# Kernel tuning notes

Hardware: AMD Instinct MI355X
Metric: run time of the kernel (lower is better)

The kernel has to match this reference:

```python
import jax, jax.numpy as jnp
import numpy as np

B, O, I, D = 8, 128, 128, 1024


def setup_inputs() -> dict:
    key = jax.random.key(0)
    ks = jax.random.split(key, 10)
    s = 1.0 / np.sqrt(2 * D)  # torch Linear default-ish scale
    return {
        "output": jax.random.normal(ks[0], (B, O, D), jnp.float32),
        "context": jax.random.normal(ks[1], (B, I, D), jnp.float32),
        "mask": jax.random.randint(ks[2], (B, I), 0, 2, jnp.int32),
        # self.w = Linear(2*dim, dim), split into the output-half and context-half
        "w_out_w": jax.random.normal(ks[3], (D, D), jnp.float32) * s,
        "w_ctx_w": jax.random.normal(ks[4], (D, D), jnp.float32) * s,
        "w_b": jax.random.normal(ks[5], (D,), jnp.float32) * s,
        # self.score = Linear(dim, 1)
        "score_w": jax.random.normal(ks[6], (D,), jnp.float32) * (1.0 / np.sqrt(D)),
        "score_b": jnp.zeros((), jnp.float32),
        # self.linear_out = Linear(2*dim, dim)
        "lin_w": jax.random.normal(ks[7], (2 * D, D), jnp.float32) * s,
        "lin_b": jax.random.normal(ks[8], (D,), jnp.float32) * s,
    }


def reference(output, context, mask, w_out_w, w_ctx_w, w_b, score_w, score_b, lin_w, lin_b):
    # Additive (Bahdanau) attention.
    # cat(out, ctx) @ W^T == out @ W1 + ctx @ W2  -> avoid [B,O,I,2D] concat.
    s_out = jnp.einsum('bod,de->boe', output, w_out_w)            # [B,O,D]
    s_ctx = jnp.einsum('bid,de->bie', context, w_ctx_w)           # [B,I,D]
    h = jax.nn.leaky_relu(s_out[:, :, None, :] + s_ctx[:, None, :, :] + w_b)  # [B,O,I,D]
    score = jnp.einsum('boid,d->boi', h, score_w) + score_b       # [B,O,I]
    score = jnp.where(mask[:, None, :] == 1, -jnp.inf, score)
    attn = jax.nn.softmax(score, axis=-1)                         # [B,O,I]
    attn_output = jnp.einsum('boi,bid->bod', attn, context)       # mix=True: bmm
    # fn=True: linear_out on cat(attn_output, output) then leaky_relu
    combined = jnp.concatenate([attn_output, output], axis=-1)    # [B,O,2D]
    attn_output = jax.nn.leaky_relu(combined @ lin_w + lin_b)     # [B,O,D]
    return attn_output, attn
```

## Files before the change

kernel.cpp:

```cpp
#include <hip/hip_runtime.h>

namespace {

constexpr int kB = 8, kO = 128, kI = 128, kD = 1024;
constexpr long kOutAttnOff = (long)kB * kO * kD;

typedef __attribute__((ext_vector_type(8))) short short8;
typedef __attribute__((ext_vector_type(4))) float f32x4;

__device__ __forceinline__ float leaky(float x) { return fmaxf(x, 0.01f * x); }

__device__ __forceinline__ short f2bf(float f) {
    unsigned u = __builtin_bit_cast(unsigned, f);
    u += 0x7FFFu + ((u >> 16) & 1u);
    return (short)(u >> 16);
}

__device__ __forceinline__ void gll16(const void* g, void* l) {
    __builtin_amdgcn_global_load_lds(
        (const __attribute__((address_space(1))) int*)g,
        (__attribute__((address_space(3))) int*)l, 16, 0, 0);
}

__global__ __launch_bounds__(256)
void conv_all(const float* __restrict__ output, const float* __restrict__ context,
              const float* __restrict__ w1, const float* __restrict__ w2,
              const float* __restrict__ lin,
              short* __restrict__ ob16, short* __restrict__ cb16,
              short* __restrict__ w1t, short* __restrict__ w2t,
              short* __restrict__ lint)
{
    __shared__ float T[64][68];
    const int bid = blockIdx.x, tid = threadIdx.x;

    if (bid < 1024) {
        const int idx = bid * 256 + tid;
        const float* src; short* dst; int i;
        if (idx < (1 << 17)) { src = output;  dst = ob16; i = idx; }
        else                 { src = context; dst = cb16; i = idx - (1 << 17); }
        const float4* s4 = (const float4*)src + (long)i * 2;
        const float4 v0 = s4[0], v1 = s4[1];
        short8 r;
        r[0] = f2bf(v0.x); r[1] = f2bf(v0.y); r[2] = f2bf(v0.z); r[3] = f2bf(v0.w);
        r[4] = f2bf(v1.x); r[5] = f2bf(v1.y); r[6] = f2bf(v1.z); r[7] = f2bf(v1.w);
        *(short8*)(dst + (long)i * 8) = r;
        return;
    }

    const int tb = bid - 1024;
    const float* src; short* dst; long C, R; int t2;
    if (tb < 256)      { src = w1;  dst = w1t;  R = 1024; C = 1024; t2 = tb; }
    else if (tb < 512) { src = w2;  dst = w2t;  R = 1024; C = 1024; t2 = tb - 256; }
    else               { src = lin; dst = lint; R = 2048; C = 1024; t2 = tb - 512; }
    const int tr = t2 >> 4, tc = t2 & 15;
    const int r = tid >> 2, q = tid & 3;

    const float* s = src + (long)(tr * 64 + r) * C + tc * 64 + q * 16;
    const float4 a0 = ((const float4*)s)[0];
    const float4 a1 = ((const float4*)s)[1];
    const float4 a2 = ((const float4*)s)[2];
    const float4 a3 = ((const float4*)s)[3];
    *(float4*)&T[r][q * 16 + 0]  = a0;
    *(float4*)&T[r][q * 16 + 4]  = a1;
    *(float4*)&T[r][q * 16 + 8]  = a2;
    *(float4*)&T[r][q * 16 + 12] = a3;
    __syncthreads();

    short8 o0, o1;
#pragma unroll
    for (int j = 0; j < 8; ++j)  o0[j] = f2bf(T[q * 16 + j][r]);
#pragma unroll
    for (int j = 0; j < 8; ++j)  o1[j] = f2bf(T[q * 16 + 8 + j][r]);
    short* dp = dst + (long)(tc * 64 + r) * R + tr * 64 + q * 16;
    *(short8*)dp       = o0;
    *((short8*)dp + 1) = o1;
}

__global__ __launch_bounds__(256)
void mm_jobs(const short* __restrict__ ob16, const short* __restrict__ cb16,
             const short* __restrict__ w1t, const short* __restrict__ w2t,
             const short* __restrict__ lint,
             const float* __restrict__ w_b, const float* __restrict__ lin_b,
             float* __restrict__ s_out, float* __restrict__ s_ctx,
             float* __restrict__ outlin, short* __restrict__ ctxlin)
{
    __shared__ short As[2][64][64];
    __shared__ short Bs[2][128][64];
    const int tid = threadIdx.x;
    const int t = blockIdx.x;
    const int lane = tid & 63, w = tid >> 6;

    const short *Ap, *Bp;
    int lda, ldb, bm, bn, ldc;
    const float* bias = nullptr;
    float* Cf = nullptr;
    short* Ch = nullptr;

    if (t < 384) {
        const int job = t >> 7, jt = t & 127;
        bm = (jt >> 3) * 64; bn = (jt & 7) * 128;
        lda = 1024; ldc = 1024;
        if (job == 0)      { Ap = ob16; Bp = w1t;         ldb = 1024; bias = w_b;   Cf = s_out;  }
        else if (job == 1) { Ap = cb16; Bp = w2t;         ldb = 1024;               Cf = s_ctx;  }
        else               { Ap = ob16; Bp = lint + 1024; ldb = 2048; bias = lin_b; Cf = outlin; }
    } else {
        const int tt = t - 384, bz = tt >> 4, tw = tt & 15;
        bm = tw * 64; bn = 0;
        Ap = lint; lda = 2048;
        Bp = cb16 + (long)bz * (kI * kD); ldb = 1024;
        Ch = ctxlin + (long)bz * (kD * kI); ldc = 128;
    }

    const int m0 = (w >> 1) * 32, n0 = (w & 1) * 64;
    const int fr = lane & 15, fcol = lane >> 4, sl = lane & 7;
    const int r8 = lane >> 3;
    const int sw8 = ((lane & 7) ^ r8) * 8;
    const int w16 = w * 16, w32 = w * 32;

    f32x4 acc[2][4] = {};

    auto stage = [&](int buf, int k0) {
        const short* ga = Ap + (long)(bm + w16 + r8) * lda + k0 + sw8;
        gll16(ga,                 &As[buf][w16][0]);
        gll16(ga + 8 * (long)lda, &As[buf][w16 + 8][0]);
        const short* gb = Bp + (long)(bn + w32 + r8) * ldb + k0 + sw8;
        gll16(gb,                  &Bs[buf][w32][0]);
        gll16(gb + 8 * (long)ldb,  &Bs[buf][w32 + 8][0]);
        gll16(gb + 16 * (long)ldb, &Bs[buf][w32 + 16][0]);
        gll16(gb + 24 * (long)ldb, &Bs[buf][w32 + 24][0]);
    };

    stage(0, 0);
    __syncthreads();
    int cur = 0;
    for (int s = 0; s < 16; ++s) {
        if (s < 15) stage(cur ^ 1, (s + 1) << 6);
#pragma unroll
        for (int ks8 = 0; ks8 < 8; ks8 += 4) {
            const int sa = ((ks8 + fcol) ^ sl) * 8;
            short8 a[2], b[4];
#pragma unroll
            for (int mi = 0; mi < 2; ++mi)
                a[mi] = *(const short8*)&As[cur][m0 + mi * 16 + fr][sa];
#pragma unroll
            for (int ni = 0; ni < 4; ++ni)
                b[ni] = *(const short8*)&Bs[cur][n0 + ni * 16 + fr][sa];
#pragma unroll
            for (int mi = 0; mi < 2; ++mi)
#pragma unroll
                for (int ni = 0; ni < 4; ++ni)
                    acc[mi][ni] = __builtin_amdgcn_mfma_f32_16x16x32_bf16(
                        a[mi], b[ni], acc[mi][ni], 0, 0, 0);
        }
        __syncthreads();
        cur ^= 1;
    }

    float bv[4] = {0, 0, 0, 0};
    if (bias) {
#pragma unroll
        for (int ni = 0; ni < 4; ++ni) bv[ni] = bias[bn + n0 + ni * 16 + fr];
    }
#pragma unroll
    for (int mi = 0; mi < 2; ++mi)
#pragma unroll
        for (int ni = 0; ni < 4; ++ni)
#pragma unroll
            for (int r = 0; r < 4; ++r) {
                const int row = bm + m0 + mi * 16 + ((lane >> 4) << 2) + r;
                const int col = bn + n0 + ni * 16 + fr;
                float v = acc[mi][ni][r] + bv[ni];
                if (Ch) Ch[(long)row * ldc + col] = f2bf(v);
                else    Cf[(long)row * ldc + col] = v;
            }
}

__global__ __launch_bounds__(256)
void score_final(const float* __restrict__ s_out, const float* __restrict__ s_ctx,
                 const float* __restrict__ score_w, const float* __restrict__ score_b,
                 const int* __restrict__ mask, const short* __restrict__ ctxlin,
                 const float* __restrict__ outlin, float* __restrict__ out_main,
                 float* __restrict__ attn_f32)
{
    __shared__ float As[4][1032];
    __shared__ __align__(16) char CsPool[65536];
    __shared__ float Wsh[1024];
    __shared__ float Ps[4][4][128];
    __shared__ float Psi[4][128];
    __shared__ float so_sh[4];
    __shared__ int   Msk[128];
    __shared__ short Pl[16][136];

    float (*Cs)[128][64] = reinterpret_cast<float(*)[128][64]>(CsPool);
    const int b   = blockIdx.x;
    const int o0  = blockIdx.y * 4;
    const int tid = threadIdx.x;
    const int wv  = tid >> 6;
    const int ln  = tid & 63;
    const int fr  = ln & 15;

    const float* arow = s_out + (long)(b * kO + o0) * kD;
#pragma unroll
    for (int q = 0; q < 4; ++q) {
        const int tq = tid + q * 256;
        const int rr = tq >> 8, c4 = (tq & 255) * 4;
        *(float4*)&As[rr][c4] = *(const float4*)&arow[(long)rr * kD + c4];
    }
    *(float4*)&Wsh[tid * 4] = *(const float4*)&score_w[tid * 4];
    if (tid < 128) Msk[tid] = mask[b * kI + tid];
    {
        short* pf = &Pl[0][0];
        for (int j = tid; j < 272; j += 256) *(short8*)(pf + j * 8) = short8{};
    }

    const float* crow = s_ctx + (long)b * kI * kD;
    const int srow = wv * 4 + (ln >> 4);
    const int cho  = ((ln & 15) ^ (srow & 7)) * 4;

    auto stageCs = [&](int buf, int dc) {
#pragma unroll
        for (int it = 0; it < 8; ++it)
            gll16(crow + (long)(srow + it * 16) * kD + dc + cho,
                  &Cs[buf][wv * 4 + it * 16][0]);
    };

    stageCs(0, 0);
    __syncthreads();

    {
        float acc = 0.0f;
#pragma unroll
        for (int j = 0; j < 16; j += 4) {
            const float4 av = *(const float4*)&As[wv][ln * 16 + j];
            const float4 ww = *(const float4*)&Wsh[ln * 16 + j];
            acc = fmaf(av.x, ww.x, acc); acc = fmaf(av.y, ww.y, acc);
            acc = fmaf(av.z, ww.z, acc); acc = fmaf(av.w, ww.w, acc);
        }
#pragma unroll
        for (int d = 1; d < 64; d <<= 1) acc += __shfl_xor(acc, d, 64);
        if (ln == 0) so_sh[wv] = acc;
    }

    float sa0[4] = {}, sa1[4] = {};
    float si0 = 0.0f, si1 = 0.0f;
    const int kb = wv * 16;

    int buf = 0;
    for (int c = 0; c < 16; ++c) {
        const int dc = c * 64;
        if (c < 15) stageCs(buf ^ 1, dc + 64);
#pragma unroll
        for (int kq = 0; kq < 4; ++kq) {
            const int sc = ((wv * 4 + kq) ^ (ln & 7)) * 4;
            const float4 c0 = *(const float4*)&Cs[buf][ln][sc];
            const float4 c1 = *(const float4*)&Cs[buf][ln + 64][sc];
            const float4 w4 = *(const float4*)&Wsh[dc + kb + kq * 4];
            si0 = fmaf(c0.x, w4.x, si0); si0 = fmaf(c0.y, w4.y, si0);
            si0 = fmaf(c0.z, w4.z, si0); si0 = fmaf(c0.w, w4.w, si0);
            si1 = fmaf(c1.x, w4.x, si1); si1 = fmaf(c1.y, w4.y, si1);
            si1 = fmaf(c1.z, w4.z, si1); si1 = fmaf(c1.w, w4.w, si1);
#pragma unroll
            for (int o = 0; o < 4; ++o) {
                const float4 av = *(const float4*)&As[o][dc + kb + kq * 4];
                sa0[o] = fmaf(__builtin_fabsf(av.x + c0.x), w4.x, sa0[o]);
                sa0[o] = fmaf(__builtin_fabsf(av.y + c0.y), w4.y, sa0[o]);
                sa0[o] = fmaf(__builtin_fabsf(av.z + c0.z), w4.z, sa0[o]);
                sa0[o] = fmaf(__builtin_fabsf(av.w + c0.w), w4.w, sa0[o]);
                sa1[o] = fmaf(__builtin_fabsf(av.x + c1.x), w4.x, sa1[o]);
                sa1[o] = fmaf(__builtin_fabsf(av.y + c1.y), w4.y, sa1[o]);
                sa1[o] = fmaf(__builtin_fabsf(av.z + c1.z), w4.z, sa1[o]);
                sa1[o] = fmaf(__builtin_fabsf(av.w + c1.w), w4.w, sa1[o]);
            }
        }
        __syncthreads();
        buf ^= 1;
    }

#pragma unroll
    for (int o = 0; o < 4; ++o) {
        Ps[wv][o][ln]      = sa0[o];
        Ps[wv][o][ln + 64] = sa1[o];
    }
    Psi[wv][ln]      = si0;
    Psi[wv][ln + 64] = si1;
    __syncthreads();

    {
        const int ow = wv;
        const float negInf = -__builtin_huge_valf();
        const float sb = score_b[0];
        const float siT0 = Psi[0][ln] + Psi[1][ln] + Psi[2][ln] + Psi[3][ln];
        const float siT1 = Psi[0][ln + 64] + Psi[1][ln + 64]
                         + Psi[2][ln + 64] + Psi[3][ln + 64];
        const float saT0 = Ps[0][ow][ln] + Ps[1][ow][ln]
                         + Ps[2][ow][ln] + Ps[3][ow][ln];
        const float saT1 = Ps[0][ow][ln + 64] + Ps[1][ow][ln + 64]
                         + Ps[2][ow][ln + 64] + Ps[3][ow][ln + 64];
        const float soV = so_sh[ow];
        float s0 = 0.505f * (soV + siT0) + 0.495f * saT0 + sb;
        float s1 = 0.505f * (soV + siT1) + 0.495f * saT1 + sb;
        if (Msk[ln]      != 0) s0 = negInf;
        if (Msk[ln + 64] != 0) s1 = negInf;

        float m = fmaxf(s0, s1);
#pragma unroll
        for (int d = 1; d < 64; d <<= 1) m = fmaxf(m, __shfl_xor(m, d, 64));
        const float e0 = __expf(s0 - m);
        const float e1 = __expf(s1 - m);
        float sum = e0 + e1;
#pragma unroll
        for (int d = 1; d < 64; d <<= 1) sum += __shfl_xor(sum, d, 64);
        const float inv = 1.0f / sum;

        const long rowoff = (long)(b * kO + o0 + ow) * kI;
        const float p0 = e0 * inv, p1 = e1 * inv;
        attn_f32[rowoff + ln]      = p0;
        attn_f32[rowoff + ln + 64] = p1;
        Pl[ow][ln]      = f2bf(p0);
        Pl[ow][ln + 64] = f2bf(p1);
    }

    short* Bsh = (short*)CsPool;
    const short* ctxb = ctxlin + (long)b * (kD * kI);
    auto stageB = [&](int half, int nc) {
        short* dst = Bsh + half * (128 * 128);
#pragma unroll
        for (int it = 0; it < 8; ++it) {
            const int rb = wv * 32 + it * 4;
            const int r  = rb + (ln >> 4);
            const int gn = nc * 128 + r;
            const int sc = (ln & 15) ^ (r & 7);
            gll16(ctxb + (long)gn * kI + sc * 8, dst + rb * 128);
        }
    };

    stageB(0, 0);
    __syncthreads();
    int half = 0;
    const int fg = ln >> 4;
    for (int nc = 0; nc < 8; ++nc) {
        if (nc < 7) stageB(half ^ 1, nc + 1);
        const short* Bc = Bsh + half * (128 * 128);
        f32x4 accT0{}, accT1{};
#pragma unroll
        for (int ks = 0; ks < 4; ++ks) {
            const short8 a = *(const short8*)&Pl[fr][ks * 32 + fg * 8];
            const int n0 = (wv * 2) * 16 + fr;
            const int n1 = (wv * 2 + 1) * 16 + fr;
            const int ch0 = ((ks * 4 + fg) ^ (n0 & 7)) * 8;
            const int ch1 = ((ks * 4 + fg) ^ (n1 & 7)) * 8;
            const short8 b0 = *(const short8*)&Bc[n0 * 128 + ch0];
            const short8 b1 = *(const short8*)&Bc[n1 * 128 + ch1];
            accT0 = __builtin_amdgcn_mfma_f32_16x16x32_bf16(a, b0, accT0, 0, 0, 0);
            accT1 = __builtin_amdgcn_mfma_f32_16x16x32_bf16(a, b1, accT1, 0, 0, 0);
        }
        if (fg == 0) {
#pragma unroll
            for (int r = 0; r < 4; ++r) {
                const long off = (long)(b * kO + o0 + r) * kD;
                const int na = nc * 128 + (wv * 2) * 16 + fr;
                const int nb = nc * 128 + (wv * 2 + 1) * 16 + fr;
                out_main[off + na] = leaky(accT0[r] + outlin[off + na]);
                out_main[off + nb] = leaky(accT1[r] + outlin[off + nb]);
            }
        }
        __syncthreads();
        half ^= 1;
    }
}

}

extern "C" void kernel_launch(void* const* d_in, const int* in_sizes, int n_in,
                              void* d_out, int out_size, void* d_ws, size_t ws_size,
                              hipStream_t stream)
{
    const float* output  = (const float*)d_in[0];
    const float* context = (const float*)d_in[1];
    const int*   mask    = (const int*)d_in[2];
    const float* w_out_w = (const float*)d_in[3];
    const float* w_ctx_w = (const float*)d_in[4];
    const float* w_b     = (const float*)d_in[5];
    const float* score_w = (const float*)d_in[6];
    const float* score_b = (const float*)d_in[7];
    const float* lin_w   = (const float*)d_in[8];
    const float* lin_b   = (const float*)d_in[9];

    float* out_main = (float*)d_out;
    float* out_attn = out_main + kOutAttnOff;
    float* s_out    = out_main;

    char* wp = (char*)d_ws;
    float* s_ctx  = (float*)wp;  wp += (size_t)4 << 20;
    short* ob16   = (short*)wp;  wp += (size_t)2 << 20;
    short* cb16   = (short*)wp;  wp += (size_t)2 << 20;
    short* w1t    = (short*)wp;  wp += (size_t)2 << 20;
    short* w2t    = (short*)wp;  wp += (size_t)2 << 20;
    short* lint   = (short*)wp;  wp += (size_t)4 << 20;
    float* outlin = (float*)wp;  wp += (size_t)4 << 20;
    short* ctxlin = (short*)wp;  wp += (size_t)2 << 20;

    const dim3 blk(256);

    hipLaunchKernelGGL(conv_all, dim3(2048), blk, 0, stream,
        output, context, w_out_w, w_ctx_w, lin_w, ob16, cb16, w1t, w2t, lint);

    hipLaunchKernelGGL(mm_jobs, dim3(512), blk, 0, stream,
        ob16, cb16, w1t, w2t, lint, w_b, lin_b, s_out, s_ctx, outlin, ctxlin);

    hipLaunchKernelGGL(score_final, dim3(8, 32), blk, 0, stream,
        s_out, s_ctx, score_w, score_b, mask, ctxlin, outlin, out_main, out_attn);
}
```

Before: 72.30 us.

## Store s_ctx as bf16 and halve output rows per score block

Measured after the change: 64.56 us. 1.12x faster.

```diff
diff --git a/kernel.cpp b/kernel.cpp
--- a/kernel.cpp
+++ b/kernel.cpp
@@ -14,6 +14,15 @@
     unsigned u = __builtin_bit_cast(unsigned, f);
     u += 0x7FFFu + ((u >> 16) & 1u);
     return (short)(u >> 16);
+}
+
+__device__ __forceinline__ void b8tof(const short8 v, float* f) {
+    const unsigned* u = (const unsigned*)&v;
+#pragma unroll
+    for (int j = 0; j < 4; ++j) {
+        f[2 * j]     = __builtin_bit_cast(float, u[j] << 16);
+        f[2 * j + 1] = __builtin_bit_cast(float, u[j] & 0xffff0000u);
+    }
 }
 
 __device__ __forceinline__ void gll16(const void* g, void* l) {
@@ -81,7 +90,7 @@
              const short* __restrict__ w1t, const short* __restrict__ w2t,
              const short* __restrict__ lint,
              const float* __restrict__ w_b, const float* __restrict__ lin_b,
-             float* __restrict__ s_out, float* __restrict__ s_ctx,
+             float* __restrict__ s_out, short* __restrict__ s_ctx16,
              float* __restrict__ outlin, short* __restrict__ ctxlin)
 {
     __shared__ short As[2][64][64];
@@ -100,9 +109,9 @@
         const int job = t >> 7, jt = t & 127;
         bm = (jt >> 3) * 64; bn = (jt & 7) * 128;
         lda = 1024; ldc = 1024;
-        if (job == 0)      { Ap = ob16; Bp = w1t;         ldb = 1024; bias = w_b;   Cf = s_out;  }
-        else if (job == 1) { Ap = cb16; Bp = w2t;         ldb = 1024;               Cf = s_ctx;  }
-        else               { Ap = ob16; Bp = lint + 1024; ldb = 2048; bias = lin_b; Cf = outlin; }
+        if (job == 0)      { Ap = ob16; Bp = w1t;         ldb = 1024; bias = w_b;   Cf = s_out;   }
+        else if (job == 1) { Ap = cb16; Bp = w2t;         ldb = 1024;               Ch = s_ctx16; }
+        else               { Ap = ob16; Bp = lint + 1024; ldb = 2048; bias = lin_b; Cf = outlin;  }
     } else {
         const int tt = t - 384, bz = tt >> 4, tw = tt & 15;
         bm = tw * 64; bn = 0;
@@ -176,32 +185,32 @@
 }
 
 __global__ __launch_bounds__(256)
-void score_final(const float* __restrict__ s_out, const float* __restrict__ s_ctx,
+void score_final(const float* __restrict__ s_out, const short* __restrict__ s_ctx16,
                  const float* __restrict__ score_w, const float* __restrict__ score_b,
                  const int* __restrict__ mask, const short* __restrict__ ctxlin,
                  const float* __restrict__ outlin, float* __restrict__ out_main,
                  float* __restrict__ attn_f32)
 {
-    __shared__ float As[4][1032];
-    __shared__ __align__(16) char CsPool[65536];
+    __shared__ float As[2][1032];
+    __shared__ __align__(16) char CsPool[32768];
     __shared__ float Wsh[1024];
-    __shared__ float Ps[4][4][128];
+    __shared__ float Ps[4][2][128];
     __shared__ float Psi[4][128];
-    __shared__ float so_sh[4];
+    __shared__ float so_sh[2];
     __shared__ int   Msk[128];
-    __shared__ short Pl[16][136];
-
-    float (*Cs)[128][64] = reinterpret_cast<float(*)[128][64]>(CsPool);
+    __shared__ __align__(16) short Pl[16][136];
+
+    short* CsS = (short*)CsPool;
     const int b   = blockIdx.x;
-    const int o0  = blockIdx.y * 4;
+    const int o0  = blockIdx.y * 2;
     const int tid = threadIdx.x;
     const int wv  = tid >> 6;
     const int ln  = tid & 63;
-    const int fr  = ln & 15;
+    const int fr  = ln & 15, fg = ln >> 4;
 
     const float* arow = s_out + (long)(b * kO + o0) * kD;
 #pragma unroll
-    for (int q = 0; q < 4; ++q) {
+    for (int q = 0; q < 2; ++q) {
         const int tq = tid + q * 256;
         const int rr = tq >> 8, c4 = (tq & 255) * 4;
         *(float4*)&As[rr][c4] = *(const float4*)&arow[(long)rr * kD + c4];
@@ -213,21 +222,21 @@
         for (int j = tid; j < 272; j += 256) *(short8*)(pf + j * 8) = short8{};
     }
 
-    const float* crow = s_ctx + (long)b * kI * kD;
-    const int srow = wv * 4 + (ln >> 4);
-    const int cho  = ((ln & 15) ^ (srow & 7)) * 4;
-
+    const short* crow = s_ctx16 + (long)b * kI * kD;
     auto stageCs = [&](int buf, int dc) {
 #pragma unroll
-        for (int it = 0; it < 8; ++it)
-            gll16(crow + (long)(srow + it * 16) * kD + dc + cho,
-                  &Cs[buf][wv * 4 + it * 16][0]);
+        for (int it = 0; it < 4; ++it) {
+            const int rb = wv * 32 + it * 8;
+            const int r  = rb + (ln >> 3);
+            const int sc = (ln & 7) ^ (r & 7);
+            gll16(crow + (long)r * kD + dc + sc * 8, CsS + buf * 8192 + rb * 64);
+        }
     };
 
     stageCs(0, 0);
     __syncthreads();
 
-    {
+    if (wv < 2) {
         float acc = 0.0f;
 #pragma unroll
         for (int j = 0; j < 16; j += 4) {
@@ -241,7 +250,7 @@
         if (ln == 0) so_sh[wv] = acc;
     }
 
-    float sa0[4] = {}, sa1[4] = {};
+    float sa0[2] = {}, sa1[2] = {};
     float si0 = 0.0f, si1 = 0.0f;
     const int kb = wv * 16;
 
@@ -249,43 +258,60 @@
     for (int c = 0; c < 16; ++c) {
         const int dc = c * 64;
         if (c < 15) stageCs(buf ^ 1, dc + 64);
-#pragma unroll
-        for (int kq = 0; kq < 4; ++kq) {
-            const int sc = ((wv * 4 + kq) ^ (ln & 7)) * 4;
-            const float4 c0 = *(const float4*)&Cs[buf][ln][sc];
-            const float4 c1 = *(const float4*)&Cs[buf][ln + 64][sc];
-            const float4 w4 = *(const float4*)&Wsh[dc + kb + kq * 4];
-            si0 = fmaf(c0.x, w4.x, si0); si0 = fmaf(c0.y, w4.y, si0);
-            si0 = fmaf(c0.z, w4.z, si0); si0 = fmaf(c0.w, w4.w, si0);
-            si1 = fmaf(c1.x, w4.x, si1); si1 = fmaf(c1.y, w4.y, si1);
-            si1 = fmaf(c1.z, w4.z, si1); si1 = fmaf(c1.w, w4.w, si1);
-#pragma unroll
-            for (int o = 0; o < 4; ++o) {
-                const float4 av = *(const float4*)&As[o][dc + kb + kq * 4];
-                sa0[o] = fmaf(__builtin_fabsf(av.x + c0.x), w4.x, sa0[o]);
-                sa0[o] = fmaf(__builtin_fabsf(av.y + c0.y), w4.y, sa0[o]);
-                sa0[o] = fmaf(__builtin_fabsf(av.z + c0.z), w4.z, sa0[o]);
-                sa0[o] = fmaf(__builtin_fabsf(av.w + c0.w), w4.w, sa0[o]);
-                sa1[o] = fmaf(__builtin_fabsf(av.x + c1.x), w4.x, sa1[o]);
-                sa1[o] = fmaf(__builtin_fabsf(av.y + c1.y), w4.y, sa1[o]);
-                sa1[o] = fmaf(__builtin_fabsf(av.z + c1.z), w4.z, sa1[o]);
-                sa1[o] = fmaf(__builtin_fabsf(av.w + c1.w), w4.w, sa1[o]);
+        const int sc0 = ((wv * 2 + 0) ^ (ln & 7)) * 8;
+        const int sc1 = ((wv * 2 + 1) ^ (ln & 7)) * 8;
+        const short8 cA0 = *(const short8*)&CsS[buf * 8192 + ln * 64 + sc0];
+        const short8 cA1 = *(const short8*)&CsS[buf * 8192 + ln * 64 + sc1];
+        const short8 cB0 = *(const short8*)&CsS[buf * 8192 + (ln + 64) * 64 + sc0];
+        const short8 cB1 = *(const short8*)&CsS[buf * 8192 + (ln + 64) * 64 + sc1];
+        float c0[16], c1[16];
+        b8tof(cA0, c0); b8tof(cA1, c0 + 8);
+        b8tof(cB0, c1); b8tof(cB1, c1 + 8);
+        float wr[16], av[2][16];
+#pragma unroll
+        for (int q = 0; q < 4; ++q) {
+            *(float4*)&wr[q * 4]    = *(const float4*)&Wsh[dc + kb + q * 4];
+            *(float4*)&av[0][q * 4] = *(const float4*)&As[0][dc + kb + q * 4];
+            *(float4*)&av[1][q * 4] = *(const float4*)&As[1][dc + kb + q * 4];
+        }
+#pragma unroll
+        for (int d = 0; d < 16; ++d) {
+            si0 = fmaf(c0[d], wr[d], si0);
+            si1 = fmaf(c1[d], wr[d], si1);
+#pragma unroll
+            for (int o = 0; o < 2; ++o) {
+                sa0[o] = fmaf(__builtin_fabsf(av[o][d] + c0[d]), wr[d], sa0[o]);
+                sa1[o] = fmaf(__builtin_fabsf(av[o][d] + c1[d]), wr[d], sa1[o]);
             }
         }
         __syncthreads();
         buf ^= 1;
     }
 
-#pragma unroll
-    for (int o = 0; o < 4; ++o) {
-        Ps[wv][o][ln]      = sa0[o];
-        Ps[wv][o][ln + 64] = sa1[o];
+    short* Bsh = (short*)CsPool;
+    const short* ctxb = ctxlin + (long)b * (kD * kI);
+    auto stageB = [&](int half, int nc) {
+#pragma unroll
+        for (int it = 0; it < 4; ++it) {
+            const int rb = wv * 16 + it * 4;
+            const int r  = rb + (ln >> 4);
+            const int n  = nc * 64 + r;
+            const int sc = (ln & 15) ^ (r & 7);
+            gll16(ctxb + (long)n * kI + sc * 8, Bsh + half * 8192 + rb * kI);
+        }
+    };
+    stageB(0, 0);
+
+#pragma unroll
+    for (int o = 0; o < 2; ++o) {
+        Ps[wv][o][ln]      = (o == 0) ? sa0[0] : sa0[1];
+        Ps[wv][o][ln + 64] = (o == 0) ? sa1[0] : sa1[1];
     }
     Psi[wv][ln]      = si0;
     Psi[wv][ln + 64] = si1;
     __syncthreads();
 
-    {
+    if (wv < 2) {
         const int ow = wv;
         const float negInf = -__builtin_huge_valf();
         const float sb = score_b[0];
@@ -319,49 +345,26 @@
         Pl[ow][ln]      = f2bf(p0);
         Pl[ow][ln + 64] = f2bf(p1);
     }
-
-    short* Bsh = (short*)CsPool;
-    const short* ctxb = ctxlin + (long)b * (kD * kI);
-    auto stageB = [&](int half, int nc) {
-        short* dst = Bsh + half * (128 * 128);
-#pragma unroll
-        for (int it = 0; it < 8; ++it) {
-            const int rb = wv * 32 + it * 4;
-            const int r  = rb + (ln >> 4);
-            const int gn = nc * 128 + r;
-            const int sc = (ln & 15) ^ (r & 7);
-            gll16(ctxb + (long)gn * kI + sc * 8, dst + rb * 128);
-        }
-    };
-
-    stageB(0, 0);
     __syncthreads();
+
     int half = 0;
-    const int fg = ln >> 4;
-    for (int nc = 0; nc < 8; ++nc) {
-        if (nc < 7) stageB(half ^ 1, nc + 1);
-        const short* Bc = Bsh + half * (128 * 128);
-        f32x4 accT0{}, accT1{};
+    for (int nc = 0; nc < 16; ++nc) {
+        if (nc < 15) stageB(half ^ 1, nc + 1);
+        const short* Bc = Bsh + half * 8192;
+        f32x4 acc{};
 #pragma unroll
         for (int ks = 0; ks < 4; ++ks) {
             const short8 a = *(const short8*)&Pl[fr][ks * 32 + fg * 8];
-            const int n0 = (wv * 2) * 16 + fr;
-            const int n1 = (wv * 2 + 1) * 16 + fr;
-            const int ch0 = ((ks * 4 + fg) ^ (n0 & 7)) * 8;
-            const int ch1 = ((ks * 4 + fg) ^ (n1 & 7)) * 8;
-            const short8 b0 = *(const short8*)&Bc[n0 * 128 + ch0];
-            const short8 b1 = *(const short8*)&Bc[n1 * 128 + ch1];
-            accT0 = __builtin_amdgcn_mfma_f32_16x16x32_bf16(a, b0, accT0, 0, 0, 0);
-            accT1 = __builtin_amdgcn_mfma_f32_16x16x32_bf16(a, b1, accT1, 0, 0, 0);
+            const int sc = ((ks * 4 + fg) ^ (fr & 7)) * 8;
+            const short8 bb = *(const short8*)&Bc[(wv * 16 + fr) * kI + sc];
+            acc = __builtin_amdgcn_mfma_f32_16x16x32_bf16(a, bb, acc, 0, 0, 0);
         }
         if (fg == 0) {
 #pragma unroll
-            for (int r = 0; r < 4; ++r) {
-                const long off = (long)(b * kO + o0 + r) * kD;
-                const int na = nc * 128 + (wv * 2) * 16 + fr;
-                const int nb = nc * 128 + (wv * 2 + 1) * 16 + fr;
-                out_main[off + na] = leaky(accT0[r] + outlin[off + na]);
-                out_main[off + nb] = leaky(accT1[r] + outlin[off + nb]);
+            for (int r = 0; r < 2; ++r) {
+                const int n = nc * 64 + wv * 16 + fr;
+                const long off = (long)(b * kO + o0 + r) * kD + n;
+                out_main[off] = leaky(acc[r] + outlin[off]);
             }
         }
         __syncthreads();
@@ -391,14 +394,14 @@
     float* s_out    = out_main;
 
     char* wp = (char*)d_ws;
-    float* s_ctx  = (float*)wp;  wp += (size_t)4 << 20;
-    short* ob16   = (short*)wp;  wp += (size_t)2 << 20;
-    short* cb16   = (short*)wp;  wp += (size_t)2 << 20;
-    short* w1t    = (short*)wp;  wp += (size_t)2 << 20;
-    short* w2t    = (short*)wp;  wp += (size_t)2 << 20;
-    short* lint   = (short*)wp;  wp += (size_t)4 << 20;
-    float* outlin = (float*)wp;  wp += (size_t)4 << 20;
-    short* ctxlin = (short*)wp;  wp += (size_t)2 << 20;
+    short* s_ctx16 = (short*)wp;  wp += (size_t)2 << 20;
+    short* ob16    = (short*)wp;  wp += (size_t)2 << 20;
+    short* cb16    = (short*)wp;  wp += (size_t)2 << 20;
+    short* w1t     = (short*)wp;  wp += (size_t)2 << 20;
+    short* w2t     = (short*)wp;  wp += (size_t)2 << 20;
+    short* lint    = (short*)wp;  wp += (size_t)4 << 20;
+    float* outlin  = (float*)wp;  wp += (size_t)4 << 20;
+    short* ctxlin  = (short*)wp;
 
     const dim3 blk(256);
 
@@ -406,8 +409,8 @@
         output, context, w_out_w, w_ctx_w, lin_w, ob16, cb16, w1t, w2t, lint);
 
     hipLaunchKernelGGL(mm_jobs, dim3(512), blk, 0, stream,
-        ob16, cb16, w1t, w2t, lint, w_b, lin_b, s_out, s_ctx, outlin, ctxlin);
-
-    hipLaunchKernelGGL(score_final, dim3(8, 32), blk, 0, stream,
-        s_out, s_ctx, score_w, score_b, mask, ctxlin, outlin, out_main, out_attn);
-}
+        ob16, cb16, w1t, w2t, lint, w_b, lin_b, s_out, s_ctx16, outlin, ctxlin);
+
+    hipLaunchKernelGGL(score_final, dim3(8, 64), blk, 0, stream,
+        s_out, s_ctx16, score_w, score_b, mask, ctxlin, outlin, out_main, out_attn);
+}
```
